# Kernel optimization log

Measured on AMD Instinct MI355X. Metric: run time of the kernel, lower is better.

Reference implementation:

```python
import jax, jax.numpy as jnp
import numpy as np

K = 256  # k winners per row


def setup_inputs() -> dict:
    key = jax.random.key(0)
    k1, k2 = jax.random.split(key)
    x = jax.random.normal(k1, (32768, 2048), dtype=jnp.float32)
    importance = jax.random.normal(k2, (2048,), dtype=jnp.float32)
    return {"x": x, "importance": importance}


def reference(x, importance):
    # scores = |x| * |importance|  (broadcast over batch)
    scores = jnp.abs(x) * jnp.abs(importance)
    # top-k indices per row, then scatter 1.0 into a zero mask
    _, idx = jax.lax.top_k(scores, K)              # [B, K]
    rows = jnp.arange(x.shape[0])[:, None]          # [B, 1]
    mask = jnp.zeros_like(x).at[rows, idx].set(1.0)
    return x * mask
```

## Files before the change

kernel.cpp:

```cpp
#include <hip/hip_runtime.h>

#define COLS 2048
#define KSEL 256
#define TPB  256
#define EPT  8

__global__ __launch_bounds__(TPB)
void CompetitiveSelection_topk_kernel(const float* __restrict__ x,
                                      const float* __restrict__ imp,
                                      float* __restrict__ out)
{
    const int row = blockIdx.x;
    const int tid = threadIdx.x;
    const long base = (long)row * COLS + (long)tid * EPT;

    __shared__ __align__(16) unsigned int hist[2304];
    __shared__ __align__(16) unsigned int bsum[256];
    __shared__ __align__(16) unsigned int tcnt[256];
    __shared__ unsigned int bc[2];

    float4 xa = *(const float4*)(x + base);
    float4 xb = *(const float4*)(x + base + 4);
    float4 ia = *(const float4*)(imp + tid * EPT);
    float4 ib = *(const float4*)(imp + tid * EPT + 4);

    float xv[EPT] = {xa.x, xa.y, xa.z, xa.w, xb.x, xb.y, xb.z, xb.w};
    float iv[EPT] = {ia.x, ia.y, ia.z, ia.w, ib.x, ib.y, ib.z, ib.w};

    unsigned int sc[EPT];
#pragma unroll
    for (int i = 0; i < EPT; ++i)
        sc[i] = __float_as_uint(fabsf(xv[i]) * fabsf(iv[i]));

    unsigned int T  = 0;
    unsigned int kk = KSEL;

    auto scan256 = [&](const unsigned int* cnts, unsigned int curT, int shift,
                       unsigned int curkk) {
        if (tid < 64) {
            uint4 v = *(const uint4*)&cnts[4 * tid];
            unsigned int cnt[4] = {v.x, v.y, v.z, v.w};
            unsigned int tot = v.x + v.y + v.z + v.w;
            unsigned int S = tot;
#pragma unroll
            for (int off = 1; off < 64; off <<= 1) {
                unsigned int u = __shfl_down(S, off);
                if (tid + off < 64) S += u;
            }
            unsigned int above = S - tot;
            int c = -1;
            unsigned int cab = 0;
#pragma unroll
            for (int b = 3; b >= 0; --b) {
                if (c < 0 && above < curkk && above + cnt[b] >= curkk) {
                    c = 4 * tid + b;
                    cab = above;
                }
                above += cnt[b];
            }
            if (c >= 0) {
                bc[0] = curT | ((unsigned int)c << shift);
                bc[1] = curkk - cab;
            }
        }
    };

    {
#pragma unroll
        for (int k = 0; k < 9; ++k) hist[tid + 256 * k] = 0;
        __syncthreads();

        const unsigned int rep = tid & 7u;
#pragma unroll
        for (int i = 0; i < EPT; i += 2) {
            unsigned int d0 = sc[i] >> 23;
            unsigned int d1 = sc[i + 1] >> 23;
            atomicAdd(&hist[9 * d0 + rep], 1u + (d0 == d1));
            if (d0 != d1) atomicAdd(&hist[9 * d1 + rep], 1u);
        }
        __syncthreads();

        unsigned int s = 0;
#pragma unroll
        for (int r = 0; r < 8; ++r) s += hist[9 * tid + r];
        bsum[tid] = s;
        __syncthreads();

        scan256(bsum, T, 23, kk);
        __syncthreads();
        T = bc[0]; kk = bc[1];
    }

    {
#pragma unroll
        for (int k = 0; k < 3; ++k) hist[tid + 256 * k] = 0;
        __syncthreads();

        const unsigned int rep = tid & 1u;
        const unsigned int hm = 0xFF800000u;
#pragma unroll
        for (int i = 0; i < EPT; ++i) {
            if ((sc[i] & hm) == T)
                atomicAdd(&hist[3 * ((sc[i] >> 15) & 255u) + rep], 1u);
        }
        __syncthreads();

        bsum[tid] = hist[3 * tid] + hist[3 * tid + 1];
        __syncthreads();

        scan256(bsum, T, 15, kk);
        __syncthreads();
        T = bc[0]; kk = bc[1];
    }

    {
        hist[tid] = 0;
        __syncthreads();

        const unsigned int hm = 0xFFFF8000u;
#pragma unroll
        for (int i = 0; i < EPT; ++i) {
            if ((sc[i] & hm) == T)
                atomicAdd(&hist[(sc[i] >> 7) & 255u], 1u);
        }
        __syncthreads();

        scan256(hist, T, 7, kk);
        __syncthreads();
        T = bc[0]; kk = bc[1];
    }

    {
        hist[tid] = 0;
        __syncthreads();

        const unsigned int hm = 0xFFFFFF80u;
#pragma unroll
        for (int i = 0; i < EPT; ++i) {
            if ((sc[i] & hm) == T)
                atomicAdd(&hist[sc[i] & 127u], 1u);
        }
        __syncthreads();

        scan256(hist, T, 0, kk);
        __syncthreads();
        T = bc[0]; kk = bc[1];
    }

    unsigned int myeq = 0;
    bool isel[EPT];
#pragma unroll
    for (int i = 0; i < EPT; ++i) {
        isel[i] = sc[i] > T;
        myeq += (sc[i] == T) ? 1u : 0u;
    }
    tcnt[tid] = myeq;
    __syncthreads();

    if (tid < 64) {
        uint4 v = *(const uint4*)&tcnt[4 * tid];
        unsigned int tot = v.x + v.y + v.z + v.w;
        unsigned int S = tot;
#pragma unroll
        for (int off = 1; off < 64; off <<= 1) {
            unsigned int u = __shfl_up(S, off);
            if (tid >= off) S += u;
        }
        unsigned int excl = S - tot;
        uint4 o;
        o.x = excl;
        o.y = o.x + v.x;
        o.z = o.y + v.y;
        o.w = o.z + v.z;
        *(uint4*)&tcnt[4 * tid] = o;
    }
    __syncthreads();
    unsigned int ebase = tcnt[tid];

    float ov[EPT];
#pragma unroll
    for (int i = 0; i < EPT; ++i) {
        bool pick = isel[i];
        if (sc[i] == T) { pick = (ebase < kk); ebase += 1; }
        ov[i] = pick ? xv[i] : 0.0f;
    }
    *(float4*)(out + base)     = make_float4(ov[0], ov[1], ov[2], ov[3]);
    *(float4*)(out + base + 4) = make_float4(ov[4], ov[5], ov[6], ov[7]);
}

extern "C" void kernel_launch(void* const* d_in, const int* in_sizes, int n_in,
                              void* d_out, int out_size, void* d_ws, size_t ws_size,
                              hipStream_t stream)
{
    const float* x   = (const float*)d_in[0];
    const float* imp = (const float*)d_in[1];
    float* out       = (float*)d_out;

    const int rows = in_sizes[0] / COLS;
    CompetitiveSelection_topk_kernel<<<dim3(rows), dim3(TPB), 0, stream>>>(x, imp, out);
}
```

Before: 108.5 us.

## Exit radix passes early and resolve small candidate sets with wave ballots

```diff
diff --git a/kernel.cpp b/kernel.cpp
--- a/kernel.cpp
+++ b/kernel.cpp
@@ -14,10 +14,9 @@
     const int tid = threadIdx.x;
     const long base = (long)row * COLS + (long)tid * EPT;
 
-    __shared__ __align__(16) unsigned int hist[2304];
+    __shared__ __align__(16) unsigned int hist[2080];
     __shared__ __align__(16) unsigned int bsum[256];
-    __shared__ __align__(16) unsigned int tcnt[256];
-    __shared__ unsigned int bc[2];
+    __shared__ unsigned int bc[4];
 
     float4 xa = *(const float4*)(x + base);
     float4 xb = *(const float4*)(x + base + 4);
@@ -32,15 +31,14 @@
     for (int i = 0; i < EPT; ++i)
         sc[i] = __float_as_uint(fabsf(xv[i]) * fabsf(iv[i]));
 
-    unsigned int T  = 0;
-    unsigned int kk = KSEL;
+    unsigned int T = 0, kk = KSEL, na = 0, ne = 0;
 
     auto scan256 = [&](const unsigned int* cnts, unsigned int curT, int shift,
                        unsigned int curkk) {
         if (tid < 64) {
-            uint4 v = *(const uint4*)&cnts[4 * tid];
-            unsigned int cnt[4] = {v.x, v.y, v.z, v.w};
-            unsigned int tot = v.x + v.y + v.z + v.w;
+            uint4 v4 = *(const uint4*)&cnts[4 * tid];
+            unsigned int cnt[4] = {v4.x, v4.y, v4.z, v4.w};
+            unsigned int tot = v4.x + v4.y + v4.z + v4.w;
             unsigned int S = tot;
 #pragma unroll
             for (int off = 1; off < 64; off <<= 1) {
@@ -48,142 +46,165 @@
                 if (tid + off < 64) S += u;
             }
             unsigned int above = S - tot;
-            int c = -1;
-            unsigned int cab = 0;
+            int c = -1; unsigned int cab = 0, cnb = 0;
 #pragma unroll
             for (int b = 3; b >= 0; --b) {
                 if (c < 0 && above < curkk && above + cnt[b] >= curkk) {
-                    c = 4 * tid + b;
-                    cab = above;
+                    c = 4 * tid + b; cab = above; cnb = cnt[b];
                 }
                 above += cnt[b];
             }
             if (c >= 0) {
                 bc[0] = curT | ((unsigned int)c << shift);
                 bc[1] = curkk - cab;
+                bc[2] = cnb;
+                bc[3] = 0;
             }
         }
     };
 
     {
-#pragma unroll
-        for (int k = 0; k < 9; ++k) hist[tid + 256 * k] = 0;
-        __syncthreads();
-
-        const unsigned int rep = tid & 7u;
-#pragma unroll
-        for (int i = 0; i < EPT; i += 2) {
-            unsigned int d0 = sc[i] >> 23;
-            unsigned int d1 = sc[i + 1] >> 23;
-            atomicAdd(&hist[9 * d0 + rep], 1u + (d0 == d1));
-            if (d0 != d1) atomicAdd(&hist[9 * d1 + rep], 1u);
+        uint4* H4 = (uint4*)hist;
+        H4[tid]       = make_uint4(0, 0, 0, 0);
+        H4[256 + tid] = make_uint4(0, 0, 0, 0);
+        if (tid < 8) H4[512 + tid] = make_uint4(0, 0, 0, 0);
+        __syncthreads();
+
+        const unsigned int rb = 260u * (tid & 7u);
+#pragma unroll
+        for (int g = 0; g < EPT; g += 4) {
+            unsigned int d0 = sc[g] >> 23, d1 = sc[g + 1] >> 23,
+                         d2 = sc[g + 2] >> 23, d3 = sc[g + 3] >> 23;
+            atomicAdd(&hist[rb + d0], 1u + (d1 == d0) + (d2 == d0) + (d3 == d0));
+            if (d1 != d0)                         atomicAdd(&hist[rb + d1], 1u + (d2 == d1) + (d3 == d1));
+            if (d2 != d0 && d2 != d1)             atomicAdd(&hist[rb + d2], 1u + (d3 == d2));
+            if (d3 != d0 && d3 != d1 && d3 != d2) atomicAdd(&hist[rb + d3], 1u);
         }
         __syncthreads();
 
         unsigned int s = 0;
 #pragma unroll
-        for (int r = 0; r < 8; ++r) s += hist[9 * tid + r];
+        for (int r = 0; r < 8; ++r) s += hist[260 * r + tid];
         bsum[tid] = s;
         __syncthreads();
 
-        scan256(bsum, T, 23, kk);
-        __syncthreads();
-        T = bc[0]; kk = bc[1];
-    }
-
-    {
-#pragma unroll
-        for (int k = 0; k < 3; ++k) hist[tid + 256 * k] = 0;
-        __syncthreads();
-
-        const unsigned int rep = tid & 1u;
-        const unsigned int hm = 0xFF800000u;
+        scan256(bsum, 0u, 23, KSEL);
+        __syncthreads();
+        T = bc[0]; kk = bc[1]; na = bc[2];
+    }
+
+    int nbits = 23;
+    unsigned int hm = 0xFF800000u;
+
+    if (na > 64) {
+        hist[tid] = 0;
+        __syncthreads();
+#pragma unroll
+        for (int i = 0; i < EPT; ++i)
+            if ((sc[i] & hm) == T) atomicAdd(&hist[(sc[i] >> 15) & 255u], 1u);
+        __syncthreads();
+        scan256(hist, T, 15, kk);
+        __syncthreads();
+        T = bc[0]; kk = bc[1]; na = bc[2];
+        nbits = 15; hm = 0xFFFF8000u;
+
+        if (na > 64) {
+            hist[tid] = 0;
+            __syncthreads();
+#pragma unroll
+            for (int i = 0; i < EPT; ++i)
+                if ((sc[i] & hm) == T) atomicAdd(&hist[(sc[i] >> 7) & 255u], 1u);
+            __syncthreads();
+            scan256(hist, T, 7, kk);
+            __syncthreads();
+            T = bc[0]; kk = bc[1]; na = bc[2];
+            nbits = 7; hm = 0xFFFFFF80u;
+
+            if (na > 64) {
+                hist[tid] = 0;
+                __syncthreads();
+#pragma unroll
+                for (int i = 0; i < EPT; ++i)
+                    if ((sc[i] & hm) == T) atomicAdd(&hist[sc[i] & 127u], 1u);
+                __syncthreads();
+                scan256(hist, T, 0, kk);
+                __syncthreads();
+                T = bc[0]; kk = bc[1]; na = bc[2];
+                nbits = 0;
+            }
+        }
+    }
+
+    if (nbits > 0) {
 #pragma unroll
         for (int i = 0; i < EPT; ++i) {
-            if ((sc[i] & hm) == T)
-                atomicAdd(&hist[3 * ((sc[i] >> 15) & 255u) + rep], 1u);
-        }
-        __syncthreads();
-
-        bsum[tid] = hist[3 * tid] + hist[3 * tid + 1];
-        __syncthreads();
-
-        scan256(bsum, T, 15, kk);
-        __syncthreads();
-        T = bc[0]; kk = bc[1];
-    }
-
-    {
-        hist[tid] = 0;
-        __syncthreads();
-
-        const unsigned int hm = 0xFFFF8000u;
+            if ((sc[i] & hm) == T) {
+                unsigned int p = atomicAdd(&bc[3], 1u);
+                bsum[p] = sc[i];
+            }
+        }
+        __syncthreads();
+        if (tid < 64) {
+            unsigned int v = (tid < (int)na) ? bsum[tid] : 0u;
+            unsigned long long M = __ballot(tid < (int)na);
+            unsigned int tl = 0, k2 = kk;
+            for (int b = nbits - 1; b >= 0; --b) {
+                unsigned long long ones = __ballot((v >> b) & 1u) & M;
+                unsigned int c1 = (unsigned int)__popcll(ones);
+                if (c1 >= k2) { M = ones; tl |= (1u << b); }
+                else          { M &= ~ones; k2 -= c1; }
+            }
+            if (tid == 0) {
+                bc[0] = T | tl;
+                bc[1] = k2;
+                bc[2] = (unsigned int)__popcll(M);
+            }
+        }
+        __syncthreads();
+        T = bc[0]; kk = bc[1]; ne = bc[2];
+    } else {
+        ne = na;
+    }
+
+    float ov[EPT];
+    if (ne == kk) {
+#pragma unroll
+        for (int i = 0; i < EPT; ++i)
+            ov[i] = (sc[i] >= T) ? xv[i] : 0.0f;
+    } else {
+        unsigned int myeq = 0;
+        bool isel[EPT];
 #pragma unroll
         for (int i = 0; i < EPT; ++i) {
-            if ((sc[i] & hm) == T)
-                atomicAdd(&hist[(sc[i] >> 7) & 255u], 1u);
-        }
-        __syncthreads();
-
-        scan256(hist, T, 7, kk);
-        __syncthreads();
-        T = bc[0]; kk = bc[1];
-    }
-
-    {
-        hist[tid] = 0;
-        __syncthreads();
-
-        const unsigned int hm = 0xFFFFFF80u;
+            isel[i] = sc[i] > T;
+            myeq += (sc[i] == T) ? 1u : 0u;
+        }
+        hist[tid] = myeq;
+        __syncthreads();
+        if (tid < 64) {
+            uint4 v = *(const uint4*)&hist[4 * tid];
+            unsigned int tot = v.x + v.y + v.z + v.w;
+            unsigned int S = tot;
+#pragma unroll
+            for (int off = 1; off < 64; off <<= 1) {
+                unsigned int u = __shfl_up(S, off);
+                if (tid >= off) S += u;
+            }
+            unsigned int excl = S - tot;
+            uint4 o;
+            o.x = excl; o.y = o.x + v.x; o.z = o.y + v.y; o.w = o.z + v.z;
+            *(uint4*)&hist[4 * tid] = o;
+        }
+        __syncthreads();
+        unsigned int ebase = hist[tid];
 #pragma unroll
         for (int i = 0; i < EPT; ++i) {
-            if ((sc[i] & hm) == T)
-                atomicAdd(&hist[sc[i] & 127u], 1u);
-        }
-        __syncthreads();
-
-        scan256(hist, T, 0, kk);
-        __syncthreads();
-        T = bc[0]; kk = bc[1];
-    }
-
-    unsigned int myeq = 0;
-    bool isel[EPT];
-#pragma unroll
-    for (int i = 0; i < EPT; ++i) {
-        isel[i] = sc[i] > T;
-        myeq += (sc[i] == T) ? 1u : 0u;
-    }
-    tcnt[tid] = myeq;
-    __syncthreads();
-
-    if (tid < 64) {
-        uint4 v = *(const uint4*)&tcnt[4 * tid];
-        unsigned int tot = v.x + v.y + v.z + v.w;
-        unsigned int S = tot;
-#pragma unroll
-        for (int off = 1; off < 64; off <<= 1) {
-            unsigned int u = __shfl_up(S, off);
-            if (tid >= off) S += u;
-        }
-        unsigned int excl = S - tot;
-        uint4 o;
-        o.x = excl;
-        o.y = o.x + v.x;
-        o.z = o.y + v.y;
-        o.w = o.z + v.z;
-        *(uint4*)&tcnt[4 * tid] = o;
-    }
-    __syncthreads();
-    unsigned int ebase = tcnt[tid];
-
-    float ov[EPT];
-#pragma unroll
-    for (int i = 0; i < EPT; ++i) {
-        bool pick = isel[i];
-        if (sc[i] == T) { pick = (ebase < kk); ebase += 1; }
-        ov[i] = pick ? xv[i] : 0.0f;
-    }
+            bool pick = isel[i];
+            if (sc[i] == T) { pick = (ebase < kk); ebase += 1; }
+            ov[i] = pick ? xv[i] : 0.0f;
+        }
+    }
+
     *(float4*)(out + base)     = make_float4(ov[0], ov[1], ov[2], ov[3]);
     *(float4*)(out + base + 4) = make_float4(ov[4], ov[5], ov[6], ov[7]);
 }
```

New measurement: 104.7 us. -3.4%, faster.
